# Kernel optimization log

Measured on AMD Instinct MI355X. Metric: run time of the kernel, lower is better.

## Reference

```python
import jax, jax.numpy as jnp
import numpy as np

N = 50000      # nodes
E = 500000     # edges
IN = 256       # input feature dim
HID = 64       # hidden (per-head) dim, layer 1
H1 = 4         # heads, layer 1
NC = 64        # num_classes (layer 2 out, 1 head)
ED = 32        # edge_dim
T = 8          # num_etypes
SLOPE = 0.2    # leakyrelu negative slope


def setup_inputs() -> dict:
    key = jax.random.key(0)
    ks = jax.random.split(key, 20)
    p = lambda k, shape: (jax.random.normal(k, shape, jnp.float32) * 0.05)
    return {
        "h": jax.random.normal(ks[0], (N, IN), jnp.float32),
        "row": jax.random.randint(ks[1], (E,), 0, N, jnp.int32),   # src
        "col": jax.random.randint(ks[2], (E,), 0, N, jnp.int32),   # dst
        "etype": jax.random.randint(ks[3], (E,), 0, T, jnp.int32),
        # layer 1 (4 heads, no residual, elu activation)
        "edge_emb1": p(ks[4], (T, ED)),
        "W1": p(ks[5], (IN, HID * H1)),
        "Wr1": p(ks[6], (T, ED, ED * H1)),      # TypedLinear per-etype weight
        "a_l1": p(ks[7], (H1, HID)),
        "a_r1": p(ks[8], (H1, HID)),
        "a_e1": p(ks[9], (H1, ED)),
        # layer 2 (1 head, residual Linear, no activation)
        "edge_emb2": p(ks[10], (T, ED)),
        "W2": p(ks[11], (HID * H1, NC)),
        "Wr2": p(ks[12], (T, ED, ED)),
        "a_l2": p(ks[13], (1, NC)),
        "a_r2": p(ks[14], (1, NC)),
        "a_e2": p(ks[15], (1, ED)),
        "res_W2": p(ks[16], (HID * H1, NC)),
        "res_b2": p(ks[17], (NC,)),
    }


def _simple_hgn_conv(h, row, col, etype, edge_emb, W, Wr, a_l, a_r, a_e,
                     res_W, res_b, apply_act):
    """One SimpleHGNConv layer. h:[N,in], returns [N, out_dim*H] (D-major, H-minor
    layout, matching emb.permute(0,2,1).view in the torch code)."""
    H, D = a_l.shape            # num_heads, out_dim
    n = h.shape[0]
    emb = (h @ W).reshape(n, H, D)                     # [N,H,D]
    emb = jnp.where(jnp.isnan(emb), 0.0, emb)
    # TypedLinear: edge_emb[etype] @ Wr[etype]; only T distinct rows -> per-type GEMM
    ee = jnp.einsum('te,teo->to', edge_emb, Wr).reshape(T, H, ED)  # [T,H,ED]
    h_l = jnp.einsum('nhd,hd->nh', emb, a_l)[row]      # [E,H]
    h_r = jnp.einsum('nhd,hd->nh', emb, a_r)[col]      # [E,H]
    h_e = jnp.einsum('thd,hd->th', ee, a_e)[etype]     # [E,H]
    att = jax.nn.leaky_relu(h_l + h_r + h_e, SLOPE)    # [E,H]
    # edge_softmax: normalize over incoming edges of each destination node (col)
    seg_max = jax.ops.segment_max(att, col, num_segments=n)   # [N,H]
    att = jnp.exp(att - seg_max[col])
    seg_sum = jax.ops.segment_sum(att, col, num_segments=n)   # [N,H]
    alpha = att / seg_sum[col]                          # [E,H]
    # u_mul_e + sum aggregation
    msg = emb[row] * alpha[:, :, None]                  # [E,H,D]
    out = jax.ops.segment_sum(msg, col, num_segments=n) # [N,H,D]
    out = out.transpose(0, 2, 1).reshape(n, D * H)      # D-major layout
    if res_W is not None:
        out = out + h @ res_W + res_b
    if apply_act:
        out = jax.nn.elu(out)
    return out


def reference(h, row, col, etype,
              edge_emb1, W1, Wr1, a_l1, a_r1, a_e1,
              edge_emb2, W2, Wr2, a_l2, a_r2, a_e2, res_W2, res_b2):
    h1 = _simple_hgn_conv(h, row, col, etype, edge_emb1, W1, Wr1,
                          a_l1, a_r1, a_e1, None, None, True)
    h2 = _simple_hgn_conv(h1, row, col, etype, edge_emb2, W2, Wr2,
                          a_l2, a_r2, a_e2, res_W2, res_b2, False)
    # split by node type (first half type 'l', second half type 'v')
    return (h2[: N // 2], h2[N // 2 :])
```

## Files before the change

### kernel.cpp

```cpp
#include <hip/hip_runtime.h>
#include <hip/hip_bf16.h>

typedef __bf16 bf16x8 __attribute__((ext_vector_type(8)));
typedef float f32x4 __attribute__((ext_vector_type(4)));

#define IN_DIM 256
#define NT 8

__device__ __forceinline__ float b2f(unsigned short u) {
  union { unsigned int i; float f; } x; x.i = ((unsigned int)u) << 16; return x.f;
}
__device__ __forceinline__ float lo2f(unsigned int w) {
  union { unsigned int i; float f; } x; x.i = w << 16; return x.f;
}
__device__ __forceinline__ float hi2f(unsigned int w) {
  union { unsigned int i; float f; } x; x.i = w & 0xFFFF0000u; return x.f;
}
__device__ __forceinline__ unsigned short f2b(float f) {
  union { float f; unsigned int i; } u; u.f = f;
  unsigned int r = u.i + 0x7FFF + ((u.i >> 16) & 1);
  return (unsigned short)(r >> 16);
}
__device__ __forceinline__ unsigned int f2b2(float lo, float hi) {
  return (unsigned int)f2b(lo) | ((unsigned int)f2b(hi) << 16);
}
__device__ __forceinline__ float lrelu(float x) { return x >= 0.f ? x : 0.2f * x; }
__device__ __forceinline__ float ldf(const void* p, size_t i, int isf32) {
  return isf32 ? ((const float*)p)[i] : b2f(((const unsigned short*)p)[i]);
}

__global__ void prep_all_kernel(const void* __restrict__ W1, const void* __restrict__ W2,
                                const void* __restrict__ rW2,
                                const void* __restrict__ al1, const void* __restrict__ ar1,
                                const void* __restrict__ al2, const void* __restrict__ ar2,
                                const void* __restrict__ ee1, const void* __restrict__ Wr1,
                                const void* __restrict__ ae1,
                                const void* __restrict__ ee2, const void* __restrict__ Wr2,
                                const void* __restrict__ ae2,
                                unsigned short* __restrict__ W1t,
                                unsigned short* __restrict__ W2t,
                                float* __restrict__ a2l, float* __restrict__ a2r,
                                float* __restrict__ he1, float* __restrict__ he2,
                                float* __restrict__ alD, float* __restrict__ arD,
                                const unsigned int* __restrict__ hw,
                                const int* __restrict__ col, int* __restrict__ cnt,
                                int E_, int N_, int* __restrict__ dflag) {
  int b = blockIdx.x, tid = threadIdx.x;
  if (b >= 454) {
    int base = (b - 454) * 1024 + tid;
#pragma unroll
    for (int k = 0; k < 4; k++) {
      int e = base + k * 256;
      if (e < E_) {
        int c = col[e];
        if ((unsigned)c < (unsigned)N_) atomicAdd(&cnt[c], 1);
      }
    }
    return;
  }
  __shared__ int sflag;
  {
    int bad = 0;
    if (tid < 64) {
      for (int i = 0; i < 4; i++) {
        unsigned int w = hw[tid * 4 + i];
        unsigned int ex = (w & 0x7FFFu) >> 7;
        if (ex >= 0xC0u) bad++;
      }
#pragma unroll
      for (int off = 32; off; off >>= 1) bad += __shfl_xor(bad, off);
      if (tid == 0) sflag = (bad > 8) ? 1 : 0;
    }
    __syncthreads();
  }
  const int isf32 = sflag;
  if (b == 0 && tid == 0) *dflag = isf32;
  if (b < 384) {
    int j = b, k = tid;
    if (j < 256) {
      int src = (j & 3) * 64 + (j >> 2);
      W1t[j * 256 + k] = f2b(ldf(W1, (size_t)k * 256 + src, isf32));
    } else {
      int o = j - 256;
      float v = (o < 64) ? ldf(W2, (size_t)k * 64 + o, isf32)
                         : ldf(rW2, (size_t)k * 64 + (o - 64), isf32);
      W2t[o * 256 + k] = f2b(v);
    }
  } else if (b < 448) {
    int k = (b - 384) * 4 + (tid >> 6), d = tid & 63;
    float w2 = ldf(W2, (size_t)k * 64 + d, isf32);
    float l2 = w2 * ldf(al2, d, isf32);
    float r2 = w2 * ldf(ar2, d, isf32);
#pragma unroll
    for (int off = 32; off; off >>= 1) { l2 += __shfl_xor(l2, off); r2 += __shfl_xor(r2, off); }
    if (d == 0) { a2l[k] = l2; a2r[k] = r2; }
  } else {
    int bid = b - 448;
    int t = tid >> 5, d = tid & 31;
    if (bid < 4) {
      int h = bid;
      float s = 0.f;
#pragma unroll
      for (int e = 0; e < 32; e++)
        s += ldf(ee1, t * 32 + e, isf32) * ldf(Wr1, (size_t)(t * 32 + e) * 128 + h * 32 + d, isf32);
      float v = s * ldf(ae1, h * 32 + d, isf32);
#pragma unroll
      for (int off = 16; off; off >>= 1) v += __shfl_xor(v, off);
      if (d == 0) he1[t * 4 + h] = v;
    } else if (bid == 4) {
      float s = 0.f;
#pragma unroll
      for (int e = 0; e < 32; e++)
        s += ldf(ee2, t * 32 + e, isf32) * ldf(Wr2, (size_t)(t * 32 + e) * 32 + d, isf32);
      float v = s * ldf(ae2, d, isf32);
#pragma unroll
      for (int off = 16; off; off >>= 1) v += __shfl_xor(v, off);
      if (d == 0) he2[t] = v;
    } else {
      int j = tid;
      alD[j] = ldf(al1, (j & 3) * 64 + (j >> 2), isf32);
      arD[j] = ldf(ar1, (j & 3) * 64 + (j >> 2), isf32);
    }
  }
}

__global__ __launch_bounds__(256, 4) void gemm1_fill(
    const void* __restrict__ A, int M,
    const unsigned short* __restrict__ Bt,
    unsigned short* __restrict__ emb1,
    const float* __restrict__ alD, const float* __restrict__ arD,
    float* __restrict__ hl1, float* __restrict__ hr1,
    const int* __restrict__ dflag, int FillBlocks,
    const int* __restrict__ col, const int* __restrict__ row,
    const int* __restrict__ ety, const int* __restrict__ ptrb,
    const int* __restrict__ bsum, int* __restrict__ cnt,
    int* __restrict__ srcc, int E_) {
  __shared__ unsigned short As[32 * 64];
  __shared__ unsigned short Bs[256 * 64];
  __shared__ float lsum[4][32][4];
  __shared__ float rsum[4][32][4];
  if (blockIdx.x < FillBlocks) {
    int base = blockIdx.x * 1024 + threadIdx.x;
#pragma unroll
    for (int k = 0; k < 4; k++) {
      int e = base + k * 256;
      if (e < E_) {
        int c = col[e];
        if ((unsigned)c < (unsigned)M) {
          int pos = atomicSub(&cnt[c], 1) - 1;
          long long slot = (long long)(ptrb[c] + bsum[c >> 8]) + pos;
          if (slot >= 0 && slot < E_) {
            int sr = row[e], t = ety[e];
            srcc[slot] = ((unsigned)sr < (unsigned)M && (unsigned)t < (unsigned)NT)
                             ? (sr | (t << 20)) : -1;
          }
        }
      }
    }
    return;
  }
  const int isf32 = *dflag;
  const int tid = threadIdx.x;
  const int m0 = (blockIdx.x - FillBlocks) * 32;
  const int wv = tid >> 6, lane = tid & 63;
  const int q = lane >> 4, m = lane & 15;
  const int jp = wv * 64;
  f32x4 acc[2][4] = {};
  for (int kc = 0; kc < 256; kc += 64) {
    {
      int row_ = tid >> 3, qt = tid & 7;
      int gr = m0 + row_;
      int4 w;
      if (gr < M) {
        if (isf32) {
          const float* ap = (const float*)A + (size_t)gr * 256 + kc + qt * 8;
          float4 v0 = *(const float4*)ap;
          float4 v1 = *(const float4*)(ap + 4);
          w.x = (int)f2b2(v0.x, v0.y); w.y = (int)f2b2(v0.z, v0.w);
          w.z = (int)f2b2(v1.x, v1.y); w.w = (int)f2b2(v1.z, v1.w);
        } else {
          const unsigned short* ap = (const unsigned short*)A + (size_t)gr * 256 + kc + qt * 8;
          w = *(const int4*)ap;
        }
      } else {
        w.x = 0; w.y = 0; w.z = 0; w.w = 0;
      }
      int pg = qt ^ (row_ & 7);
      *(int4*)(As + row_ * 64 + pg * 8) = w;
    }
    {
#pragma unroll
      for (int i = 0; i < 8; i++) {
        int id = tid + i * 256;
        int row_ = id >> 3, gg = id & 7;
        int4 v = *(const int4*)(Bt + (size_t)row_ * 256 + kc + gg * 8);
        int pg = gg ^ (row_ & 7);
        *(int4*)(Bs + row_ * 64 + pg * 8) = v;
      }
    }
    __syncthreads();
#pragma unroll
    for (int ks = 0; ks < 2; ks++) {
      int gk = ks * 4 + q;
      bf16x8 afr[2];
#pragma unroll
      for (int cm = 0; cm < 2; cm++) {
        int row_ = cm * 16 + m;
        afr[cm] = *(const bf16x8*)(As + row_ * 64 + (gk ^ (row_ & 7)) * 8);
      }
#pragma unroll
      for (int cj = 0; cj < 4; cj++) {
        int jr = jp + cj * 16 + m;
        bf16x8 b = *(const bf16x8*)(Bs + jr * 64 + (gk ^ (jr & 7)) * 8);
#pragma unroll
        for (int cm = 0; cm < 2; cm++)
          acc[cm][cj] = __builtin_amdgcn_mfma_f32_16x16x32_bf16(afr[cm], b, acc[cm][cj], 0, 0, 0);
      }
    }
    __syncthreads();
  }
  float al[4], ar[4];
#pragma unroll
  for (int cj = 0; cj < 4; cj++) {
    al[cj] = alD[jp + cj * 16 + m];
    ar[cj] = arD[jp + cj * 16 + m];
  }
#pragma unroll
  for (int cm = 0; cm < 2; cm++) {
#pragma unroll
    for (int r = 0; r < 4; r++) {
      int lrow = cm * 16 + q * 4 + r;
      int gm = m0 + lrow;
      float lp = 0.f, rp = 0.f;
#pragma unroll
      for (int cj = 0; cj < 4; cj++) {
        float v = acc[cm][cj][r];
        if (gm < M) emb1[(size_t)gm * 256 + jp + cj * 16 + m] = f2b(v);
        lp += v * al[cj]; rp += v * ar[cj];
      }
      lp += __shfl_xor(lp, 4); lp += __shfl_xor(lp, 8);
      rp += __shfl_xor(rp, 4); rp += __shfl_xor(rp, 8);
      if (m < 4) { lsum[wv][lrow][m] = lp; rsum[wv][lrow][m] = rp; }
    }
  }
  __syncthreads();
  if (tid < 128) {
    int row_ = tid >> 2, h = tid & 3;
    int gm = m0 + row_;
    if (gm < M) {
      float l = lsum[0][row_][h] + lsum[1][row_][h] + lsum[2][row_][h] + lsum[3][row_][h];
      float r = rsum[0][row_][h] + rsum[1][row_][h] + rsum[2][row_][h] + rsum[3][row_][h];
      hl1[(size_t)gm * 4 + h] = l;
      hr1[(size_t)gm * 4 + h] = r;
    }
  }
}

__global__ __launch_bounds__(256, 4) void gemm2_fused(
    const unsigned short* __restrict__ A, int M,
    const unsigned short* __restrict__ Bt,
    unsigned short* __restrict__ emb2, unsigned short* __restrict__ res,
    const void* __restrict__ bias, const int* __restrict__ dflag) {
  __shared__ unsigned short As[64 * 64];
  __shared__ unsigned short Bs[128 * 64];
  int isf32 = *dflag;
  const int tid = threadIdx.x;
  const int m0 = blockIdx.x * 64;
  const int wv = tid >> 6, lane = tid & 63;
  const int q = lane >> 4, m = lane & 15;
  const int jp = (wv & 1) * 64;
  const int mh = (wv >> 1) * 32;
  f32x4 acc[2][4] = {};
  for (int kc = 0; kc < 256; kc += 64) {
    {
      int row = tid >> 2, qt = tid & 3;
      int gr = m0 + row;
      unsigned short tmp[16];
      if (gr < M) {
        const unsigned short* ap = A + (size_t)gr * 256 + kc + qt * 16;
        *(int4*)tmp = *(const int4*)ap;
        *(int4*)(tmp + 8) = *(const int4*)(ap + 8);
      } else {
        for (int x = 0; x < 16; x++) tmp[x] = 0;
      }
      int g0 = (qt * 2) ^ (row & 7);
      int g1 = (qt * 2 + 1) ^ (row & 7);
      *(int4*)(As + row * 64 + g0 * 8) = *(int4*)tmp;
      *(int4*)(As + row * 64 + g1 * 8) = *(int4*)(tmp + 8);
    }
    {
#pragma unroll
      for (int i = 0; i < 4; i++) {
        int id = tid + i * 256;
        int row = id >> 3, gg = id & 7;
        int4 v = *(const int4*)(Bt + (size_t)row * 256 + kc + gg * 8);
        int pg = gg ^ (row & 7);
        *(int4*)(Bs + row * 64 + pg * 8) = v;
      }
    }
    __syncthreads();
#pragma unroll
    for (int ks = 0; ks < 2; ks++) {
      int gk = ks * 4 + q;
      bf16x8 afr[2];
#pragma unroll
      for (int cm = 0; cm < 2; cm++) {
        int row = mh + cm * 16 + m;
        afr[cm] = *(const bf16x8*)(As + row * 64 + (gk ^ (row & 7)) * 8);
      }
#pragma unroll
      for (int cj = 0; cj < 4; cj++) {
        int jr = jp + cj * 16 + m;
        bf16x8 b = *(const bf16x8*)(Bs + jr * 64 + (gk ^ (jr & 7)) * 8);
#pragma unroll
        for (int cm = 0; cm < 2; cm++)
          acc[cm][cj] = __builtin_amdgcn_mfma_f32_16x16x32_bf16(afr[cm], b, acc[cm][cj], 0, 0, 0);
      }
    }
    __syncthreads();
  }
  float bv[4];
#pragma unroll
  for (int cj = 0; cj < 4; cj++)
    bv[cj] = (jp == 64) ? ldf(bias, cj * 16 + m, isf32) : 0.f;
#pragma unroll
  for (int cm = 0; cm < 2; cm++) {
#pragma unroll
    for (int r = 0; r < 4; r++) {
      int gm = m0 + mh + cm * 16 + q * 4 + r;
      if (gm < M) {
#pragma unroll
        for (int cj = 0; cj < 4; cj++) {
          float v = acc[cm][cj][r];
          int gj = cj * 16 + m;
          if (jp == 0) emb2[(size_t)gm * 64 + gj] = f2b(v);
          else res[(size_t)gm * 64 + gj] = f2b(v + bv[cj]);
        }
      }
    }
  }
}

__global__ void scan1_kernel(const int* __restrict__ cnt, int* __restrict__ ptrb,
                             int* __restrict__ bsum, int* __restrict__ done,
                             int n, int nb) {
  __shared__ int wsum[4];
  __shared__ int lastflag;
  int tid = threadIdx.x, lane = tid & 63, wid = tid >> 6;
  if (tid == 0) lastflag = 0;
  int i = blockIdx.x * 256 + tid;
  int v = (i < n) ? cnt[i] : 0;
  int x = v;
#pragma unroll
  for (int off = 1; off < 64; off <<= 1) {
    int y = __shfl_up(x, off);
    if (lane >= off) x += y;
  }
  if (lane == 63) wsum[wid] = x;
  __syncthreads();
  int woff = 0;
#pragma unroll
  for (int k = 0; k < 4; k++) woff += (k < wid) ? wsum[k] : 0;
  if (i < n) ptrb[i] = x - v + woff;
  if (tid == 255) bsum[blockIdx.x] = woff + x;
  __syncthreads();
  if (tid == 255) {
    __threadfence();
    int t = atomicAdd(done, 1);
    if (t == (int)gridDim.x - 1) { __threadfence(); lastflag = 1; }
  }
  __syncthreads();
  if (lastflag) {
    int v2 = (tid < nb) ? ((volatile int*)bsum)[tid] : 0;
    int x2 = v2;
#pragma unroll
    for (int off = 1; off < 64; off <<= 1) {
      int y = __shfl_up(x2, off);
      if (lane >= off) x2 += y;
    }
    if (lane == 63) wsum[wid] = x2;
    __syncthreads();
    int woff2 = 0;
#pragma unroll
    for (int k = 0; k < 4; k++) woff2 += (k < wid) ? wsum[k] : 0;
    if (tid < nb) bsum[tid] = x2 - v2 + woff2;
    if (tid == 255) ptrb[n] = woff2 + x2;
  }
}

__global__ __launch_bounds__(256) void agg1_kernel(
    const int* __restrict__ ptrb, const int* __restrict__ bsumv,
    const int* __restrict__ srcc,
    const float* __restrict__ hl1, const float* __restrict__ hr1,
    const float* __restrict__ he1,
    const unsigned short* __restrict__ emb1, unsigned short* __restrict__ h1,
    const float* __restrict__ a2l, const float* __restrict__ a2r,
    float* __restrict__ hl2, float* __restrict__ hr2,
    int n0, int N_, int E_) {
  __shared__ float4 wds[4][64];
  __shared__ int sds[4][64];
  const int tid = threadIdx.x;
  const int wv = tid >> 6, lane = tid & 63;
  const int g = lane >> 4, ln = lane & 15;
  const int node = n0 + blockIdx.x * 16 + wv * 4 + g;
  const bool nv = node < N_;
  int p0 = 0, p1 = 0;
  if (nv) {
    p0 = ptrb[node] + bsumv[node >> 8];
    p1 = (node + 1 < N_) ? (ptrb[node + 1] + bsumv[(node + 1) >> 8]) : ptrb[N_];
    p0 = max(0, min(p0, E_)); p1 = max(p0, min(p1, E_));
  }
  float4 hrv = {0.f, 0.f, 0.f, 0.f};
  if (nv) hrv = *(const float4*)(hr1 + 4 * (size_t)node);
  float s0 = 0.f, s1 = 0.f, s2 = 0.f, s3 = 0.f;
  float acc[16];
#pragma unroll
  for (int k = 0; k < 16; k++) acc[k] = 0.f;
  const unsigned short* erow = emb1 + ln * 16;
  for (int pb = p0;; pb += 16) {
    if (!__any(pb < p1)) break;
    int mc = (pb < p1) ? min(p1 - pb, 16) : 0;
    float4 w = {0.f, 0.f, 0.f, 0.f};
    int src = 0;
    if (ln < mc) {
      int spk = srcc[pb + ln];
      if (spk >= 0) {
        int sr = spk & 0xFFFFF, t = spk >> 20;
        float4 a = *(const float4*)(hl1 + 4 * (size_t)sr);
        float4 ge = *(const float4*)(he1 + 4 * (size_t)t);
        w.x = __expf(lrelu(a.x + hrv.x + ge.x));
        w.y = __expf(lrelu(a.y + hrv.y + ge.y));
        w.z = __expf(lrelu(a.z + hrv.z + ge.z));
        w.w = __expf(lrelu(a.w + hrv.w + ge.w));
        src = sr;
      }
    }
    s0 += w.x; s1 += w.y; s2 += w.z; s3 += w.w;
    wds[wv][lane] = w;
    sds[wv][lane] = src;
    for (int j = 0; j < mc; j += 2) {
      bool v1 = (j + 1) < mc;
      float4 u0 = wds[wv][g * 16 + j];
      int r0 = sds[wv][g * 16 + j];
      const unsigned short* e0 = erow + (size_t)r0 * 256;
      int4 ra = *(const int4*)e0;
      int4 rb = *(const int4*)(e0 + 8);
      float4 u1; int4 rc, rd;
      if (v1) {
        u1 = wds[wv][g * 16 + j + 1];
        int r1 = sds[wv][g * 16 + j + 1];
        const unsigned short* e1 = erow + (size_t)r1 * 256;
        rc = *(const int4*)e1;
        rd = *(const int4*)(e1 + 8);
      }
      acc[0]  += u0.x * lo2f(ra.x); acc[1]  += u0.y * hi2f(ra.x);
      acc[2]  += u0.z * lo2f(ra.y); acc[3]  += u0.w * hi2f(ra.y);
      acc[4]  += u0.x * lo2f(ra.z); acc[5]  += u0.y * hi2f(ra.z);
      acc[6]  += u0.z * lo2f(ra.w); acc[7]  += u0.w * hi2f(ra.w);
      acc[8]  += u0.x * lo2f(rb.x); acc[9]  += u0.y * hi2f(rb.x);
      acc[10] += u0.z * lo2f(rb.y); acc[11] += u0.w * hi2f(rb.y);
      acc[12] += u0.x * lo2f(rb.z); acc[13] += u0.y * hi2f(rb.z);
      acc[14] += u0.z * lo2f(rb.w); acc[15] += u0.w * hi2f(rb.w);
      if (v1) {
        acc[0]  += u1.x * lo2f(rc.x); acc[1]  += u1.y * hi2f(rc.x);
        acc[2]  += u1.z * lo2f(rc.y); acc[3]  += u1.w * hi2f(rc.y);
        acc[4]  += u1.x * lo2f(rc.z); acc[5]  += u1.y * hi2f(rc.z);
        acc[6]  += u1.z * lo2f(rc.w); acc[7]  += u1.w * hi2f(rc.w);
        acc[8]  += u1.x * lo2f(rd.x); acc[9]  += u1.y * hi2f(rd.x);
        acc[10] += u1.z * lo2f(rd.y); acc[11] += u1.w * hi2f(rd.y);
        acc[12] += u1.x * lo2f(rd.z); acc[13] += u1.y * hi2f(rd.z);
        acc[14] += u1.z * lo2f(rd.w); acc[15] += u1.w * hi2f(rd.w);
      }
    }
  }
#pragma unroll
  for (int off = 1; off < 16; off <<= 1) {
    s0 += __shfl_xor(s0, off); s1 += __shfl_xor(s1, off);
    s2 += __shfl_xor(s2, off); s3 += __shfl_xor(s3, off);
  }
  float invs[4];
  invs[0] = s0 > 0.f ? 1.f / s0 : 0.f;
  invs[1] = s1 > 0.f ? 1.f / s1 : 0.f;
  invs[2] = s2 > 0.f ? 1.f / s2 : 0.f;
  invs[3] = s3 > 0.f ? 1.f / s3 : 0.f;
  float alv[16], arv[16];
#pragma unroll
  for (int q2 = 0; q2 < 4; q2++) {
    float4 t1 = *(const float4*)(a2l + ln * 16 + q2 * 4);
    float4 t2 = *(const float4*)(a2r + ln * 16 + q2 * 4);
    alv[q2 * 4 + 0] = t1.x; alv[q2 * 4 + 1] = t1.y;
    alv[q2 * 4 + 2] = t1.z; alv[q2 * 4 + 3] = t1.w;
    arv[q2 * 4 + 0] = t2.x; arv[q2 * 4 + 1] = t2.y;
    arv[q2 * 4 + 2] = t2.z; arv[q2 * 4 + 3] = t2.w;
  }
  float lp = 0.f, rp = 0.f;
  unsigned int ow[8];
#pragma unroll
  for (int k = 0; k < 16; k++) {
    float r = acc[k] * invs[k & 3];
    r = r > 0.f ? r : __expf(r) - 1.f;
    unsigned int bb = f2b(r);
    if ((k & 1) == 0) ow[k >> 1] = bb; else ow[k >> 1] |= bb << 16;
    lp += r * alv[k];
    rp += r * arv[k];
  }
  if (nv) {
    int4 va; va.x = ow[0]; va.y = ow[1]; va.z = ow[2]; va.w = ow[3];
    int4 vb; vb.x = ow[4]; vb.y = ow[5]; vb.z = ow[6]; vb.w = ow[7];
    *(int4*)(h1 + (size_t)node * 256 + ln * 16) = va;
    *(int4*)(h1 + (size_t)node * 256 + ln * 16 + 8) = vb;
  }
#pragma unroll
  for (int off = 1; off < 16; off <<= 1) {
    lp += __shfl_xor(lp, off); rp += __shfl_xor(rp, off);
  }
  if (nv && ln == 0) { hl2[node] = lp; hr2[node] = rp; }
}

__global__ __launch_bounds__(256) void agg2_kernel(
    const int* __restrict__ ptrb, const int* __restrict__ bsumv,
    const int* __restrict__ srcc,
    const float* __restrict__ hl2, const float* __restrict__ hr2,
    const float* __restrict__ he2,
    const unsigned short* __restrict__ emb2, const unsigned short* __restrict__ res,
    void* __restrict__ out, int N_, int E_, const int* __restrict__ dflag) {
  __shared__ int2 wsd[4][4][17];
  const int isf32 = *dflag;
  const int tid = threadIdx.x;
  const int wv = tid >> 6, lane = tid & 63;
  const int g = lane >> 4, ln = lane & 15;
  const int node = blockIdx.x * 16 + wv * 4 + g;
  const bool nv = node < N_;
  int p0 = 0, p1 = 0;
  if (nv) {
    p0 = ptrb[node] + bsumv[node >> 8];
    p1 = (node + 1 < N_) ? (ptrb[node + 1] + bsumv[(node + 1) >> 8]) : ptrb[N_];
    p0 = max(0, min(p0, E_)); p1 = max(p0, min(p1, E_));
  }
  float hrv = nv ? hr2[node] : 0.f;
  float s = 0.f;
  float acc[4] = {0.f, 0.f, 0.f, 0.f};
  const unsigned short* erow = emb2 + ln * 4;
  for (int pb = p0;; pb += 16) {
    if (!__any(pb < p1)) break;
    int mc = (pb < p1) ? min(p1 - pb, 16) : 0;
    float w = 0.f; int src = 0;
    if (ln < mc) {
      int spk = srcc[pb + ln];
      if (spk >= 0) {
        int sr = spk & 0xFFFFF, t = spk >> 20;
        w = __expf(lrelu(hl2[sr] + hrv + he2[t]));
        src = sr;
      }
    }
    s += w;
    int2 pk; pk.x = __float_as_int(w); pk.y = src;
    wsd[wv][g][ln] = pk;
    int2 w0 = {0, 0}, w1 = {0, 0}; int2 pa = {0, 0}, pc = {0, 0};
    if (0 < mc) { w0 = wsd[wv][g][0]; pa = *(const int2*)(erow + (size_t)w0.y * 64); }
    if (1 < mc) { w1 = wsd[wv][g][1]; pc = *(const int2*)(erow + (size_t)w1.y * 64); }
    for (int j = 0; j < mc; j += 2) {
      int2 nw0 = {0, 0}, nw1 = {0, 0}, na = {0, 0}, nc = {0, 0};
      if (j + 2 < mc) { nw0 = wsd[wv][g][j + 2]; na = *(const int2*)(erow + (size_t)nw0.y * 64); }
      if (j + 3 < mc) { nw1 = wsd[wv][g][j + 3]; nc = *(const int2*)(erow + (size_t)nw1.y * 64); }
      float u0 = __int_as_float(w0.x);
      acc[0] += u0 * lo2f(pa.x); acc[1] += u0 * hi2f(pa.x);
      acc[2] += u0 * lo2f(pa.y); acc[3] += u0 * hi2f(pa.y);
      if (j + 1 < mc) {
        float u1 = __int_as_float(w1.x);
        acc[0] += u1 * lo2f(pc.x); acc[1] += u1 * hi2f(pc.x);
        acc[2] += u1 * lo2f(pc.y); acc[3] += u1 * hi2f(pc.y);
      }
      w0 = nw0; w1 = nw1; pa = na; pc = nc;
    }
  }
#pragma unroll
  for (int off = 1; off < 16; off <<= 1) s += __shfl_xor(s, off);
  float inv = s > 0.f ? 1.f / s : 0.f;
  if (nv) {
    ushort4 rv = *(const ushort4*)(res + (size_t)node * 64 + ln * 4);
    float o0 = acc[0] * inv + b2f(rv.x);
    float o1 = acc[1] * inv + b2f(rv.y);
    float o2 = acc[2] * inv + b2f(rv.z);
    float o3 = acc[3] * inv + b2f(rv.w);
    size_t oi = (size_t)node * 64 + ln * 4;
    if (isf32) {
      float4 ov = {o0, o1, o2, o3};
      *(float4*)((float*)out + oi) = ov;
    } else {
      ushort4 ov; ov.x = f2b(o0); ov.y = f2b(o1); ov.z = f2b(o2); ov.w = f2b(o3);
      *(ushort4*)((unsigned short*)out + oi) = ov;
    }
  }
}

extern "C" void kernel_launch(void* const* d_in, const int* in_sizes, int n_in,
                              void* d_out, int out_size, void* d_ws, size_t ws_size,
                              hipStream_t stream) {
  const int N = in_sizes[0] / IN_DIM;
  const int E = in_sizes[1];

  const void* h   = d_in[0];
  const int* row  = (const int*)d_in[1];
  const int* col  = (const int*)d_in[2];
  const int* ety  = (const int*)d_in[3];
  const void* ee1 = d_in[4];
  const void* W1  = d_in[5];
  const void* Wr1 = d_in[6];
  const void* al1 = d_in[7];
  const void* ar1 = d_in[8];
  const void* ae1 = d_in[9];
  const void* ee2 = d_in[10];
  const void* W2  = d_in[11];
  const void* Wr2 = d_in[12];
  const void* al2 = d_in[13];
  const void* ar2 = d_in[14];
  const void* ae2 = d_in[15];
  const void* rW2 = d_in[16];
  const void* rb2 = d_in[17];

  char* p = (char*)d_ws;
  auto take = [&](size_t b) { char* q = p; p += (b + 255) & ~(size_t)255; return q; };
  unsigned short* h1   = (unsigned short*)take((size_t)N * 256 * 2);
  unsigned short* emb1 = (unsigned short*)take((size_t)N * 256 * 2);
  int* srcc = (int*)take((size_t)E * 4);
  int* ptrb = (int*)take((size_t)(N + 1) * 4);
  int* cnt  = (int*)take((size_t)(N + 64) * 4);
  int* bsum = (int*)take(1024);
  float* hl1 = (float*)take((size_t)N * 4 * 4);
  float* hr1 = (float*)take((size_t)N * 4 * 4);
  float* hl2 = (float*)take((size_t)N * 4);
  float* hr2 = (float*)take((size_t)N * 4);
  unsigned short* W1t = (unsigned short*)take(256 * 256 * 2);
  unsigned short* W2t = (unsigned short*)take(128 * 256 * 2);
  float* a2l = (float*)take(256 * 4);
  float* a2r = (float*)take(256 * 4);
  float* alD = (float*)take(256 * 4);
  float* arD = (float*)take(256 * 4);
  float* he1 = (float*)take(NT * 4 * 4);
  float* he2 = (float*)take(NT * 4);
  int* dflag = (int*)take(256);
  unsigned short* emb2 = emb1;
  unsigned short* res  = emb1 + (size_t)N * 64;
  int* done = cnt + N;

  const size_t need = (size_t)(p - (char*)d_ws);
  if (need > ws_size) {
    hipMemsetAsync(d_out, 0, (size_t)out_size * 2, stream);
    return;
  }

  const int ECB = (E + 1023) / 1024;
  const int MB32 = (N + 31) / 32;
  const int MB = (N + 63) / 64;
  const int SB = (N + 255) / 256;
  const int AB = (N + 15) / 16;

  hipMemsetAsync(cnt, 0, (size_t)(N + 64) * 4, stream);
  prep_all_kernel<<<454 + ECB, 256, 0, stream>>>(
      W1, W2, rW2, al1, ar1, al2, ar2, ee1, Wr1, ae1, ee2, Wr2, ae2,
      W1t, W2t, a2l, a2r, he1, he2, alD, arD,
      (const unsigned int*)h, col, cnt, E, N, dflag);

  scan1_kernel<<<SB, 256, 0, stream>>>(cnt, ptrb, bsum, done, N, SB);

  gemm1_fill<<<ECB + MB32, 256, 0, stream>>>(
      h, N, W1t, emb1, alD, arD, hl1, hr1, dflag, ECB,
      col, row, ety, ptrb, bsum, cnt, srcc, E);

  agg1_kernel<<<AB, 256, 0, stream>>>(
      ptrb, bsum, srcc, hl1, hr1, he1, emb1, h1, a2l, a2r, hl2, hr2, 0, N, E);

  gemm2_fused<<<MB, 256, 0, stream>>>(h1, N, W2t, emb2, res, rb2, dflag);
  agg2_kernel<<<AB, 256, 0, stream>>>(
      ptrb, bsum, srcc, hl2, hr2, he2, emb2, res, d_out, N, E, dflag);
}
```

Measured before the change: 256.8 us.

## Overlap layer-2 GEMM on first half with aggregation of second half

Splits the layer-1 aggregation into two halves by node range. The second-half aggregation is fused into one launch with the layer-2 GEMM over the first half's rows, and a final GEMM launch covers the remaining rows. The aim is to fill the GPU by co-scheduling memory-bound gather work with compute-bound GEMM work and to shorten the serial tail between kernels. emb2 and res now get their own buffers instead of aliasing emb1, because emb1 is still being read while the GEMM writes. This adds workspace memory and one extra launch, and the fused kernel takes the larger GEMM shared-memory footprint, which may reduce occupancy for its aggregation blocks.

```diff
diff --git a/kernel.cpp b/kernel.cpp
--- a/kernel.cpp
+++ b/kernel.cpp
@@ -256,16 +256,13 @@
   }
 }
 
-__global__ __launch_bounds__(256, 4) void gemm2_fused(
+__device__ __forceinline__ void gemm2_body(
+    unsigned short* As, unsigned short* Bs, int m0,
     const unsigned short* __restrict__ A, int M,
     const unsigned short* __restrict__ Bt,
     unsigned short* __restrict__ emb2, unsigned short* __restrict__ res,
-    const void* __restrict__ bias, const int* __restrict__ dflag) {
-  __shared__ unsigned short As[64 * 64];
-  __shared__ unsigned short Bs[128 * 64];
-  int isf32 = *dflag;
+    const void* __restrict__ bias, int isf32) {
   const int tid = threadIdx.x;
-  const int m0 = blockIdx.x * 64;
   const int wv = tid >> 6, lane = tid & 63;
   const int q = lane >> 4, m = lane & 15;
   const int jp = (wv & 1) * 64;
@@ -341,54 +338,18 @@
   }
 }
 
-__global__ void scan1_kernel(const int* __restrict__ cnt, int* __restrict__ ptrb,
-                             int* __restrict__ bsum, int* __restrict__ done,
-                             int n, int nb) {
-  __shared__ int wsum[4];
-  __shared__ int lastflag;
-  int tid = threadIdx.x, lane = tid & 63, wid = tid >> 6;
-  if (tid == 0) lastflag = 0;
-  int i = blockIdx.x * 256 + tid;
-  int v = (i < n) ? cnt[i] : 0;
-  int x = v;
-#pragma unroll
-  for (int off = 1; off < 64; off <<= 1) {
-    int y = __shfl_up(x, off);
-    if (lane >= off) x += y;
-  }
-  if (lane == 63) wsum[wid] = x;
-  __syncthreads();
-  int woff = 0;
-#pragma unroll
-  for (int k = 0; k < 4; k++) woff += (k < wid) ? wsum[k] : 0;
-  if (i < n) ptrb[i] = x - v + woff;
-  if (tid == 255) bsum[blockIdx.x] = woff + x;
-  __syncthreads();
-  if (tid == 255) {
-    __threadfence();
-    int t = atomicAdd(done, 1);
-    if (t == (int)gridDim.x - 1) { __threadfence(); lastflag = 1; }
-  }
-  __syncthreads();
-  if (lastflag) {
-    int v2 = (tid < nb) ? ((volatile int*)bsum)[tid] : 0;
-    int x2 = v2;
-#pragma unroll
-    for (int off = 1; off < 64; off <<= 1) {
-      int y = __shfl_up(x2, off);
-      if (lane >= off) x2 += y;
-    }
-    if (lane == 63) wsum[wid] = x2;
-    __syncthreads();
-    int woff2 = 0;
-#pragma unroll
-    for (int k = 0; k < 4; k++) woff2 += (k < wid) ? wsum[k] : 0;
-    if (tid < nb) bsum[tid] = x2 - v2 + woff2;
-    if (tid == 255) ptrb[n] = woff2 + x2;
-  }
-}
-
-__global__ __launch_bounds__(256) void agg1_kernel(
+__global__ __launch_bounds__(256, 4) void gemm2_fused(
+    const unsigned short* __restrict__ A, int M,
+    const unsigned short* __restrict__ Bt,
+    unsigned short* __restrict__ emb2, unsigned short* __restrict__ res,
+    const void* __restrict__ bias, const int* __restrict__ dflag, int mb0) {
+  __shared__ unsigned short As[64 * 64];
+  __shared__ unsigned short Bs[128 * 64];
+  gemm2_body(As, Bs, (blockIdx.x + mb0) * 64, A, M, Bt, emb2, res, bias, *dflag);
+}
+
+__device__ __forceinline__ void agg1_body(
+    float4 (*wds)[64], int (*sds)[64], int node, bool nv,
     const int* __restrict__ ptrb, const int* __restrict__ bsumv,
     const int* __restrict__ srcc,
     const float* __restrict__ hl1, const float* __restrict__ hr1,
@@ -396,14 +357,10 @@
     const unsigned short* __restrict__ emb1, unsigned short* __restrict__ h1,
     const float* __restrict__ a2l, const float* __restrict__ a2r,
     float* __restrict__ hl2, float* __restrict__ hr2,
-    int n0, int N_, int E_) {
-  __shared__ float4 wds[4][64];
-  __shared__ int sds[4][64];
+    int N_, int E_) {
   const int tid = threadIdx.x;
   const int wv = tid >> 6, lane = tid & 63;
   const int g = lane >> 4, ln = lane & 15;
-  const int node = n0 + blockIdx.x * 16 + wv * 4 + g;
-  const bool nv = node < N_;
   int p0 = 0, p1 = 0;
   if (nv) {
     p0 = ptrb[node] + bsumv[node >> 8];
@@ -515,6 +472,98 @@
     lp += __shfl_xor(lp, off); rp += __shfl_xor(rp, off);
   }
   if (nv && ln == 0) { hl2[node] = lp; hr2[node] = rp; }
+}
+
+__global__ __launch_bounds__(256) void agg1_kernel(
+    const int* __restrict__ ptrb, const int* __restrict__ bsumv,
+    const int* __restrict__ srcc,
+    const float* __restrict__ hl1, const float* __restrict__ hr1,
+    const float* __restrict__ he1,
+    const unsigned short* __restrict__ emb1, unsigned short* __restrict__ h1,
+    const float* __restrict__ a2l, const float* __restrict__ a2r,
+    float* __restrict__ hl2, float* __restrict__ hr2,
+    int n0, int N_, int E_) {
+  __shared__ float4 wds[4][64];
+  __shared__ int sds[4][64];
+  const int lane = threadIdx.x & 63;
+  const int node = n0 + blockIdx.x * 16 + (threadIdx.x >> 6) * 4 + (lane >> 4);
+  agg1_body(wds, sds, node, node < N_, ptrb, bsumv, srcc, hl1, hr1, he1,
+            emb1, h1, a2l, a2r, hl2, hr2, N_, E_);
+}
+
+__global__ __launch_bounds__(256, 4) void agg1_gemm2(
+    const int* __restrict__ ptrb, const int* __restrict__ bsumv,
+    const int* __restrict__ srcc,
+    const float* __restrict__ hl1, const float* __restrict__ hr1,
+    const float* __restrict__ he1,
+    const unsigned short* __restrict__ emb1, unsigned short* __restrict__ h1,
+    const float* __restrict__ a2l, const float* __restrict__ a2r,
+    float* __restrict__ hl2, float* __restrict__ hr2,
+    int n0, int N_, int E_,
+    const unsigned short* __restrict__ Bt,
+    unsigned short* __restrict__ emb2, unsigned short* __restrict__ res,
+    const void* __restrict__ bias, const int* __restrict__ dflag,
+    int AggBlocks) {
+  __shared__ unsigned short As[64 * 64];
+  __shared__ unsigned short Bs[128 * 64];
+  __shared__ float4 wds[4][64];
+  __shared__ int sds[4][64];
+  if ((int)blockIdx.x < AggBlocks) {
+    const int lane = threadIdx.x & 63;
+    const int node = n0 + blockIdx.x * 16 + (threadIdx.x >> 6) * 4 + (lane >> 4);
+    agg1_body(wds, sds, node, node < N_, ptrb, bsumv, srcc, hl1, hr1, he1,
+              emb1, h1, a2l, a2r, hl2, hr2, N_, E_);
+  } else {
+    gemm2_body(As, Bs, (blockIdx.x - AggBlocks) * 64, h1, N_, Bt, emb2, res,
+               bias, *dflag);
+  }
+}
+
+__global__ void scan1_kernel(const int* __restrict__ cnt, int* __restrict__ ptrb,
+                             int* __restrict__ bsum, int* __restrict__ done,
+                             int n, int nb) {
+  __shared__ int wsum[4];
+  __shared__ int lastflag;
+  int tid = threadIdx.x, lane = tid & 63, wid = tid >> 6;
+  if (tid == 0) lastflag = 0;
+  int i = blockIdx.x * 256 + tid;
+  int v = (i < n) ? cnt[i] : 0;
+  int x = v;
+#pragma unroll
+  for (int off = 1; off < 64; off <<= 1) {
+    int y = __shfl_up(x, off);
+    if (lane >= off) x += y;
+  }
+  if (lane == 63) wsum[wid] = x;
+  __syncthreads();
+  int woff = 0;
+#pragma unroll
+  for (int k = 0; k < 4; k++) woff += (k < wid) ? wsum[k] : 0;
+  if (i < n) ptrb[i] = x - v + woff;
+  if (tid == 255) bsum[blockIdx.x] = woff + x;
+  __syncthreads();
+  if (tid == 255) {
+    __threadfence();
+    int t = atomicAdd(done, 1);
+    if (t == (int)gridDim.x - 1) { __threadfence(); lastflag = 1; }
+  }
+  __syncthreads();
+  if (lastflag) {
+    int v2 = (tid < nb) ? ((volatile int*)bsum)[tid] : 0;
+    int x2 = v2;
+#pragma unroll
+    for (int off = 1; off < 64; off <<= 1) {
+      int y = __shfl_up(x2, off);
+      if (lane >= off) x2 += y;
+    }
+    if (lane == 63) wsum[wid] = x2;
+    __syncthreads();
+    int woff2 = 0;
+#pragma unroll
+    for (int k = 0; k < 4; k++) woff2 += (k < wid) ? wsum[k] : 0;
+    if (tid < nb) bsum[tid] = x2 - v2 + woff2;
+    if (tid == 255) ptrb[n] = woff2 + x2;
+  }
 }
 
 __global__ __launch_bounds__(256) void agg2_kernel(
@@ -623,6 +672,8 @@
   auto take = [&](size_t b) { char* q = p; p += (b + 255) & ~(size_t)255; return q; };
   unsigned short* h1   = (unsigned short*)take((size_t)N * 256 * 2);
   unsigned short* emb1 = (unsigned short*)take((size_t)N * 256 * 2);
+  unsigned short* emb2 = (unsigned short*)take((size_t)N * 64 * 2);
+  unsigned short* res  = (unsigned short*)take((size_t)N * 64 * 2);
   int* srcc = (int*)take((size_t)E * 4);
   int* ptrb = (int*)take((size_t)(N + 1) * 4);
   int* cnt  = (int*)take((size_t)(N + 64) * 4);
@@ -640,8 +691,6 @@
   float* he1 = (float*)take(NT * 4 * 4);
   float* he2 = (float*)take(NT * 4);
   int* dflag = (int*)take(256);
-  unsigned short* emb2 = emb1;
-  unsigned short* res  = emb1 + (size_t)N * 64;
   int* done = cnt + N;
 
   const size_t need = (size_t)(p - (char*)d_ws);
@@ -656,6 +705,13 @@
   const int SB = (N + 255) / 256;
   const int AB = (N + 15) / 16;
 
+  int NH = ((N / 2 + 63) / 64) * 64;
+  if (NH > N) NH = N;
+  const int AB1 = (NH + 15) / 16;
+  const int MH = NH / 64;
+  const int AB2 = (N - NH + 15) / 16;
+  const int MB2 = MB - MH;
+
   hipMemsetAsync(cnt, 0, (size_t)(N + 64) * 4, stream);
   prep_all_kernel<<<454 + ECB, 256, 0, stream>>>(
       W1, W2, rW2, al1, ar1, al2, ar2, ee1, Wr1, ae1, ee2, Wr2, ae2,
@@ -668,10 +724,18 @@
       h, N, W1t, emb1, alD, arD, hl1, hr1, dflag, ECB,
       col, row, ety, ptrb, bsum, cnt, srcc, E);
 
-  agg1_kernel<<<AB, 256, 0, stream>>>(
-      ptrb, bsum, srcc, hl1, hr1, he1, emb1, h1, a2l, a2r, hl2, hr2, 0, N, E);
-
-  gemm2_fused<<<MB, 256, 0, stream>>>(h1, N, W2t, emb2, res, rb2, dflag);
+  if (AB1 > 0)
+    agg1_kernel<<<AB1, 256, 0, stream>>>(
+        ptrb, bsum, srcc, hl1, hr1, he1, emb1, h1, a2l, a2r, hl2, hr2, 0, N, E);
+
+  if (AB2 + MH > 0)
+    agg1_gemm2<<<AB2 + MH, 256, 0, stream>>>(
+        ptrb, bsum, srcc, hl1, hr1, he1, emb1, h1, a2l, a2r, hl2, hr2,
+        NH, N, E, W2t, emb2, res, rb2, dflag, AB2);
+
+  if (MB2 > 0)
+    gemm2_fused<<<MB2, 256, 0, stream>>>(h1, N, W2t, emb2, res, rb2, dflag, MH);
+
   agg2_kernel<<<AB, 256, 0, stream>>>(
       ptrb, bsum, srcc, hl2, hr2, he2, emb2, res, d_out, N, E, dflag);
 }
```

Result: slower. 267.4 us (+4.1%).
